# Optimization experiments

Hardware: AMD Instinct MI355X
Metric: run time of the kernel (lower is better)

Reference implementation:

```python
import jax, jax.numpy as jnp
import numpy as np

BN_EPS = 1e-5

def setup_inputs() -> dict:
    key = jax.random.key(0)
    k1, k2, k3 = jax.random.split(key, 3)
    B, C, H, W = 8, 96, 56, 56
    Cout = 2 * C  # must equal 2*C for the BatchNorm in the original module
    x = jax.random.normal(k1, (B, C, H, W), dtype=jnp.float32)
    conv_w = jax.random.normal(k2, (Cout, 2 * C), dtype=jnp.float32) * (1.0 / np.sqrt(2 * C))
    conv_b = jax.random.normal(k3, (Cout,), dtype=jnp.float32) * 0.01
    gamma = jnp.ones((Cout,), dtype=jnp.float32)
    beta = jnp.zeros((Cout,), dtype=jnp.float32)
    return {"x": x, "conv_w": conv_w, "conv_b": conv_b, "gamma": gamma, "beta": beta}

def _forward(x, conv_w, conv_b, gamma, beta):
    B, C, H, W = x.shape
    # b c h w -> b n c, n = H*W
    q = x.reshape(B, C, H * W).transpose(0, 2, 1)
    # unscaled self-attention (q == k == v == tokens)
    att = jnp.einsum('bnc,bmc->bnm', q, q)          # [B, N, N]
    att = jax.nn.softmax(att, axis=-1)
    att = jnp.einsum('bnm,bmc->bnc', att, q)        # [B, N, C]
    att = att.transpose(0, 2, 1).reshape(B, C, H, W)
    # max-relative: x_j = max(0, x - att) since x_j starts at zeros
    x_j = jnp.maximum(x - att, 0.0)
    cat = jnp.concatenate([x, x_j], axis=1)          # [B, 2C, H, W]
    # 1x1 conv
    y = jnp.einsum('bchw,oc->bohw', cat, conv_w) + conv_b[None, :, None, None]
    # BatchNorm2d in training mode: biased batch stats over (B, H, W)
    mean = jnp.mean(y, axis=(0, 2, 3), keepdims=True)
    var = jnp.var(y, axis=(0, 2, 3), keepdims=True)
    y = (y - mean) * jax.lax.rsqrt(var + BN_EPS)
    y = y * gamma[None, :, None, None] + beta[None, :, None, None]
    # torch nn.GELU default is exact (erf) GELU
    return jax.nn.gelu(y, approximate=False)

def reference(x, conv_w, conv_b, gamma, beta):
    return _forward(x, conv_w, conv_b, gamma, beta)
```

## Files before the change

kernel.cpp:

```cpp
#include <hip/hip_runtime.h>
#include <hip/hip_bf16.h>

#define B_    8
#define C_    96
#define N_    3136
#define COUT_ 192
#define NTOK_ 25088
#define BN_EPS 1e-5f

#define CROW 200
#define BNC  (B_ * N_ * C_)
#define NSPLIT 3
#define NT98  98

#define K2_V_OFF 6144
#define K2_BUFSZ 14336

typedef __hip_bfloat16 bf16;
typedef unsigned short u16;
typedef unsigned int u32;
typedef __attribute__((ext_vector_type(8))) short short8;
typedef __attribute__((ext_vector_type(16))) float f32x16;

__device__ __forceinline__ u16 f2bf(float f) {
    union { __hip_bfloat16 h; u16 u; } cv;
    cv.h = __float2bfloat16(f);
    return cv.u;
}
__device__ __forceinline__ float bf2f(u16 v) {
    union { u16 u; __hip_bfloat16 h; } cv;
    cv.u = v;
    return __bfloat162float(cv.h);
}
__device__ __forceinline__ u32 packbf2(float lo, float hi) {
    return ((u32)f2bf(hi) << 16) | (u32)f2bf(lo);
}

__device__ __forceinline__ void gload_lds16(const void* g, void* l) {
    __builtin_amdgcn_global_load_lds((const __attribute__((address_space(1))) void*)g,
                                     (__attribute__((address_space(3))) void*)l,
                                     16, 0, 0);
}

__device__ __forceinline__ size_t foff(int t, int kc) {
    return ((size_t)t * 6 + kc) << 9;
}

__global__ __launch_bounds__(256) void transpose_split(const float* __restrict__ x,
                                                       u16* __restrict__ xf_hi,
                                                       u16* __restrict__ xf_lo,
                                                       u16* __restrict__ xc_hi,
                                                       float* __restrict__ norm2) {
    __shared__ float tile[32][33];
    __shared__ float nrm[32];
    const int nb = blockIdx.x * 32;
    const int cb = blockIdx.y * 32;
    const int b  = blockIdx.z;
    const int tid = threadIdx.x;
    const int tx = tid & 31;
    const int ty = tid >> 5;
    if (tid < 32) nrm[tid] = 0.0f;
    float psum = 0.0f;
#pragma unroll
    for (int r = 0; r < 32; r += 8) {
        size_t idx = ((size_t)b * C_ + cb + ty + r) * N_ + nb + tx;
        float v = x[idx];
        tile[ty + r][tx] = v;
        xc_hi[idx] = f2bf(v);
        psum = fmaf(v, v, psum);
    }
    __syncthreads();
    atomicAdd(&nrm[tx], psum);

    {
        const int item  = tid & 127;
        const int is_lo = tid >> 7;
        const int kc_i  = item >> 6;
        const int l     = item & 63;
        const int kcg   = (cb >> 4) + kc_i;
        union { u16 a[8]; short8 v8; } o;
#pragma unroll
        for (int j = 0; j < 8; j++) {
            float v = tile[kc_i * 16 + ((l >> 5) * 8) + j][l & 31];
            u16 h = f2bf(v);
            o.a[j] = is_lo ? f2bf(v - bf2f(h)) : h;
        }
        u16* dst = (is_lo ? xf_lo : xf_hi) +
                   ((size_t)b * NT98 * 6 << 9) + foff(nb >> 5, kcg) + l * 8;
        *(short8*)dst = o.v8;
    }
    __syncthreads();
    if (tid < 32)
        atomicAdd(&norm2[(size_t)b * N_ + nb + tid], nrm[tid]);
}

__global__ __launch_bounds__(256) void cast_w(const float* __restrict__ w,
                                              u16* __restrict__ wf_hi,
                                              u16* __restrict__ wf_lo) {
    int i = blockIdx.x * 256 + threadIdx.x;
    if (i >= COUT_ * 2 * C_) return;
    float v = w[i];
    u16 h  = f2bf(v);
    u16 lo = f2bf(v - bf2f(h));
    int o = i / (2 * C_), c = i % (2 * C_);
    int mt = o >> 5, lrow = o & 31;
    int ks = c >> 4, hi8 = (c >> 3) & 1, j = c & 7;
    size_t d = ((size_t)(mt * 12 + ks) * 64 + hi8 * 32 + lrow) * 8 + j;
    wf_hi[d] = h;
    wf_lo[d] = lo;
}

__global__ __launch_bounds__(256) void norm_max(const float* __restrict__ norm2,
                                                int* __restrict__ maxbits) {
    const int tid = blockIdx.x * 256 + threadIdx.x;
    float m = 0.0f;
    for (int i = tid; i < NTOK_; i += gridDim.x * 256) m = fmaxf(m, norm2[i]);
#pragma unroll
    for (int d = 1; d < 64; d <<= 1) m = fmaxf(m, __shfl_xor(m, d));
    if ((threadIdx.x & 63) == 0) atomicMax(maxbits, __float_as_int(m));
}

__global__ __launch_bounds__(256, 3) void flash_attn_mfma32(const u16* __restrict__ xf_hi,
                                                            const u16* __restrict__ xf_lo,
                                                            const u16* __restrict__ xc_hi,
                                                            const float* __restrict__ norm2,
                                                            const int* __restrict__ maxbits,
                                                            float* __restrict__ attT,
                                                            float* __restrict__ l_arr) {
    __shared__ __align__(16) char LDSU[2][K2_BUFSZ];
    const int b     = blockIdx.y;
    const int i0    = blockIdx.x * 128;
    const int split = blockIdx.z;
    const int kt0   = (NT98 * split) / NSPLIT;
    const int kt1   = (NT98 * (split + 1)) / NSPLIT;
    const int tid   = threadIdx.x;
    const int lane  = tid & 63;
    const int w     = tid >> 6;
    const int col   = lane & 31;
    const int g     = lane >> 5;

    const u16* fh = xf_hi + ((size_t)b * NT98 * 6 << 9);
    const u16* fl = xf_lo + ((size_t)b * NT98 * 6 << 9);
    const u16* vh = xc_hi + (size_t)b * C_ * N_;

    u32 loff[4], dofs[4];
#pragma unroll
    for (int j = 0; j < 4; j++) {
        int s = w + 4 * j;
        if (s >= 14) { loff[j] = 0; dofs[j] = 0; continue; }
        if (s < 6) {
            loff[j] = (u32)(s * 1024 + lane * 16);
            dofs[j] = (u32)(s * 1024);
        } else {
            int t = s - 6;
            int p = t * 64 + lane;
            int ch = p / 5, c = p % 5;
            if (c > 3) c = 3;
            loff[j] = (ch < 96) ? (u32)(ch * (N_ * 2) + c * 16) : 0u;
            dofs[j] = (u32)(K2_V_OFF + t * 1024);
        }
    }

    int qt = blockIdx.x * 4 + w;
    if (qt > NT98 - 1) qt = NT98 - 1;
    const int qrow  = i0 + w * 32 + col;
    const int qrowc = qrow < N_ ? qrow : N_ - 1;
    short8 qh[6], ql[6];
#pragma unroll
    for (int kc = 0; kc < 6; kc++) {
        qh[kc] = *(const short8*)&fh[foff(qt, kc) + lane * 8];
        ql[kc] = *(const short8*)&fl[foff(qt, kc) + lane * 8];
    }
    const float maxn2 = __int_as_float(*maxbits);
    const float m_i   = sqrtf(norm2[(size_t)b * N_ + qrowc] * maxn2);
    float l_acc = 0.0f;
    f32x16 O0 = {0}, O1 = {0}, O2 = {0};

    auto stage = [&](int nbuf, int kt) {
        const u32 ktK = (u32)kt * 6144u;
        const u32 ktV = (u32)kt * 64u;
#pragma unroll
        for (int j = 0; j < 4; j++) {
            int s = w + 4 * j;
            if (s >= 14) break;
            const char* sb = (s < 6) ? (const char*)fh + ktK
                                     : (const char*)vh + ktV;
            gload_lds16(sb + loff[j], (char*)&LDSU[nbuf][0] + dofs[j]);
        }
    };

    stage(0, kt0);
    __syncthreads();

    const int g16 = g * 16;
    int buf = 0;
    for (int kt = kt0; kt < kt1; kt++) {
        if (kt + 1 < kt1) stage(buf ^ 1, kt + 1);

        const char* Lb = (const char*)&LDSU[buf][0];

        short8 kl[6];
#pragma unroll
        for (int kc = 0; kc < 6; kc++)
            kl[kc] = *(const short8*)&fl[foff(kt, kc) + lane * 8];

        f32x16 S = {0};
        __builtin_amdgcn_s_setprio(1);
#pragma unroll
        for (int kc = 0; kc < 6; kc++) {
            short8 kh = *(const short8*)(Lb + kc * 1024 + lane * 16);
            S = __builtin_amdgcn_mfma_f32_32x32x16_bf16(kh, ql[kc], S, 0, 0, 0);
            S = __builtin_amdgcn_mfma_f32_32x32x16_bf16(kl[kc], qh[kc], S, 0, 0, 0);
            S = __builtin_amdgcn_mfma_f32_32x32x16_bf16(kh, qh[kc], S, 0, 0, 0);
        }
        __builtin_amdgcn_s_setprio(0);

        float p[16];
#pragma unroll
        for (int r = 0; r < 16; r++) {
            p[r] = __expf(S[r] - m_i);
            l_acc += p[r];
        }
        u32 w8[8];
#pragma unroll
        for (int q = 0; q < 8; q++) w8[q] = packbf2(p[2 * q], p[2 * q + 1]);

        __builtin_amdgcn_s_setprio(1);
#pragma unroll
        for (int kc = 0; kc < 2; kc++) {
            const int qb = kc * 4;
            u32 a0 = w8[qb + 0], a1 = w8[qb + 1];
            u32 a2 = w8[qb + 2], a3 = w8[qb + 3];
            u32 s0 = __shfl_xor((int)a0, 32), s1 = __shfl_xor((int)a1, 32);
            u32 s2 = __shfl_xor((int)a2, 32), s3 = __shfl_xor((int)a3, 32);
            union { short8 v; u32 u[4]; } Bf;
            Bf.u[0] = g ? s2 : a0;
            Bf.u[1] = g ? s3 : a1;
            Bf.u[2] = g ? a2 : s0;
            Bf.u[3] = g ? a3 : s1;
            const int vo = K2_V_OFF + col * 80 + kc * 32 + g16;
            short8 v0 = *(const short8*)(Lb + vo);
            short8 v1 = *(const short8*)(Lb + vo + 2560);
            short8 v2 = *(const short8*)(Lb + vo + 5120);
            O0 = __builtin_amdgcn_mfma_f32_32x32x16_bf16(v0, Bf.v, O0, 0, 0, 0);
            O1 = __builtin_amdgcn_mfma_f32_32x32x16_bf16(v1, Bf.v, O1, 0, 0, 0);
            O2 = __builtin_amdgcn_mfma_f32_32x32x16_bf16(v2, Bf.v, O2, 0, 0, 0);
        }
        __builtin_amdgcn_s_setprio(0);

        __syncthreads();
        buf ^= 1;
    }

    if (qrow < N_) {
        float* ab = attT + (size_t)b * C_ * N_ + qrow;
#pragma unroll
        for (int r = 0; r < 16; r++) {
            int c = (r & 3) + 8 * (r >> 2) + 4 * g;
            atomicAdd(&ab[(size_t)(c)      * N_], O0[r]);
            atomicAdd(&ab[(size_t)(c + 32) * N_], O1[r]);
            atomicAdd(&ab[(size_t)(c + 64) * N_], O2[r]);
        }
        float l_tot = l_acc + __shfl_xor(l_acc, 32);
        if (g == 0) atomicAdd(&l_arr[(size_t)b * N_ + qrow], l_tot);
    }
}

__global__ __launch_bounds__(128, 3) void conv_mfma(const float* __restrict__ x,
                                                    const float* __restrict__ attT,
                                                    const float* __restrict__ l_arr,
                                                    const u16* __restrict__ wf_hi,
                                                    const u16* __restrict__ wf_lo,
                                                    const float* __restrict__ convb,
                                                    float* __restrict__ y) {
    __shared__ u16 ch[32 * CROW];
    __shared__ u16 cl[32 * CROW];
    __shared__ float invl[32];
    const int b   = blockIdx.x / (N_ / 32);
    const int n0  = (blockIdx.x % (N_ / 32)) * 32;
    const int tid = threadIdx.x;

    if (tid < 32) invl[tid] = 1.0f / l_arr[(size_t)b * N_ + n0 + tid];
    __syncthreads();

    const float* xb = x    + (size_t)b * C_ * N_ + n0;
    const float* ab = attT + (size_t)b * C_ * N_ + n0;
    for (int e = tid; e < 32 * C_; e += 128) {
        int c = e >> 5, t = e & 31;
        float xv = xb[(size_t)c * N_ + t];
        float au = ab[(size_t)c * N_ + t];
        float xj = fmaxf(xv - au * invl[t], 0.0f);
        u16 h1 = f2bf(xv);
        ch[t * CROW + c] = h1;
        cl[t * CROW + c] = f2bf(xv - bf2f(h1));
        u16 h2 = f2bf(xj);
        ch[t * CROW + C_ + c] = h2;
        cl[t * CROW + C_ + c] = f2bf(xj - bf2f(h2));
    }
    __syncthreads();

    const int lane = tid & 63;
    const int w    = tid >> 6;
    const int col  = lane & 31;
    const int g    = lane >> 5;
    const int m0   = w * 3;

    f32x16 A[3] = {{0}, {0}, {0}};
#pragma unroll
    for (int ks = 0; ks < 12; ks++) {
        const int k0 = ks * 16;
        short8 bh = *(const short8*)&ch[col * CROW + k0 + g * 8];
        short8 bl = *(const short8*)&cl[col * CROW + k0 + g * 8];
#pragma unroll
        for (int mt = 0; mt < 3; mt++) {
            const size_t wo = (size_t)((m0 + mt) * 12 + ks) * 512 + lane * 8;
            short8 ah = *(const short8*)&wf_hi[wo];
            short8 al = *(const short8*)&wf_lo[wo];
            A[mt] = __builtin_amdgcn_mfma_f32_32x32x16_bf16(ah, bl, A[mt], 0, 0, 0);
            A[mt] = __builtin_amdgcn_mfma_f32_32x32x16_bf16(al, bh, A[mt], 0, 0, 0);
            A[mt] = __builtin_amdgcn_mfma_f32_32x32x16_bf16(ah, bh, A[mt], 0, 0, 0);
        }
    }

    float* yb = y + (size_t)b * COUT_ * N_ + n0 + col;
#pragma unroll
    for (int mt = 0; mt < 3; mt++)
#pragma unroll
        for (int r = 0; r < 16; r++) {
            int o = (m0 + mt) * 32 + (r & 3) + 8 * (r >> 2) + 4 * g;
            yb[(size_t)o * N_] = A[mt][r] + convb[o];
        }
}

__global__ __launch_bounds__(256) void bn_partial(const float* __restrict__ y,
                                                  float* __restrict__ pb) {
    const int o   = blockIdx.x;
    const int b   = blockIdx.y;
    const int tid = threadIdx.x;
    float s = 0.0f, q = 0.0f;
    const float4* p = (const float4*)(y + (size_t)(b * COUT_ + o) * N_);
    for (int i = tid; i < N_ / 4; i += 256) {
        float4 v = p[i];
        s += v.x + v.y + v.z + v.w;
        q += v.x * v.x + v.y * v.y + v.z * v.z + v.w * v.w;
    }
#pragma unroll
    for (int d = 1; d < 64; d <<= 1) {
        s += __shfl_xor(s, d);
        q += __shfl_xor(q, d);
    }
    __shared__ float wss[4], wqq[4];
    if ((tid & 63) == 0) { wss[tid >> 6] = s; wqq[tid >> 6] = q; }
    __syncthreads();
    if (tid == 0) {
        pb[b * COUT_ + o]                = wss[0] + wss[1] + wss[2] + wss[3];
        pb[B_ * COUT_ + b * COUT_ + o]   = wqq[0] + wqq[1] + wqq[2] + wqq[3];
    }
}

__global__ __launch_bounds__(192) void bn_finish(const float* __restrict__ pb,
                                                 const float* __restrict__ gamma,
                                                 const float* __restrict__ beta,
                                                 float* __restrict__ ss) {
    const int o = threadIdx.x;
    float s = 0.0f, q = 0.0f;
#pragma unroll
    for (int b = 0; b < B_; b++) {
        s += pb[b * COUT_ + o];
        q += pb[B_ * COUT_ + b * COUT_ + o];
    }
    const float invn = 1.0f / (float)NTOK_;
    float mean = s * invn;
    float var  = q * invn - mean * mean;
    float sc   = gamma[o] * rsqrtf(var + BN_EPS);
    ss[o]         = sc;
    ss[COUT_ + o] = beta[o] - mean * sc;
}

__global__ __launch_bounds__(256) void bn_gelu_out(const float* __restrict__ y,
                                                   const float* __restrict__ ss,
                                                   float* __restrict__ out) {
    const int total4 = (B_ * COUT_ * N_) / 4;
    int i = blockIdx.x * 256 + threadIdx.x;
    if (i >= total4) return;
    int base = i * 4;
    int o = (base / N_) % COUT_;
    float sc = ss[o], sh = ss[COUT_ + o];
    float4 v = *(const float4*)&y[base];
    float u0 = fmaf(v.x, sc, sh), u1 = fmaf(v.y, sc, sh);
    float u2 = fmaf(v.z, sc, sh), u3 = fmaf(v.w, sc, sh);
    const float k = 0.70710678118654752f;
    float4 g;
    g.x = 0.5f * u0 * (1.0f + erff(u0 * k));
    g.y = 0.5f * u1 * (1.0f + erff(u1 * k));
    g.z = 0.5f * u2 * (1.0f + erff(u2 * k));
    g.w = 0.5f * u3 * (1.0f + erff(u3 * k));
    *(float4*)&out[base] = g;
}

extern "C" void kernel_launch(void* const* d_in, const int* in_sizes, int n_in,
                              void* d_out, int out_size, void* d_ws, size_t ws_size,
                              hipStream_t stream) {
    const float* x     = (const float*)d_in[0];
    const float* w     = (const float*)d_in[1];
    const float* cb    = (const float*)d_in[2];
    const float* gamma = (const float*)d_in[3];
    const float* beta  = (const float*)d_in[4];

    u16* xf_hi = (u16*)d_ws;
    u16* xf_lo = xf_hi + (size_t)BNC;
    u16* xc_hi = xf_lo + (size_t)BNC;
    float* attT  = (float*)(xc_hi + (size_t)BNC);
    u16* wf_hi = (u16*)(attT + (size_t)BNC);
    u16* wf_lo = wf_hi + COUT_ * 2 * C_;
    float* y     = (float*)(wf_lo + COUT_ * 2 * C_);
    float* ss    = y + (size_t)B_ * COUT_ * N_;
    float* l_arr = ss + 2 * COUT_;
    float* norm2 = l_arr + NTOK_;
    int*   maxb  = (int*)(norm2 + NTOK_);
    float* pb    = attT;

    hipMemsetAsync(l_arr, 0, (2 * NTOK_) * sizeof(float) + sizeof(int), stream);
    hipMemsetAsync(attT, 0, (size_t)BNC * sizeof(float), stream);

    transpose_split<<<dim3(N_ / 32, C_ / 32, B_), 256, 0, stream>>>(x, xf_hi, xf_lo, xc_hi, norm2);
    cast_w<<<dim3((COUT_ * 2 * C_ + 255) / 256), 256, 0, stream>>>(w, wf_hi, wf_lo);
    norm_max<<<dim3(25), 256, 0, stream>>>(norm2, maxb);
    flash_attn_mfma32<<<dim3((N_ + 127) / 128, B_, NSPLIT), 256, 0, stream>>>(
        xf_hi, xf_lo, xc_hi, norm2, maxb, attT, l_arr);
    conv_mfma<<<dim3(B_ * (N_ / 32)), 128, 0, stream>>>(x, attT, l_arr, wf_hi, wf_lo, cb, y);
    bn_partial<<<dim3(COUT_, B_), 256, 0, stream>>>(y, pb);
    bn_finish<<<dim3(1), 192, 0, stream>>>(pb, gamma, beta, ss);
    bn_gelu_out<<<dim3((B_ * COUT_ * N_ / 4 + 255) / 256), 256, 0, stream>>>(y, ss, (float*)d_out);
}
```

Baseline: 206.3 us.

## Stream-K split attention tiles evenly across a fixed grid of blocks

Replaces the fixed 3-way key split per query block with a stream-K style schedule. 768 blocks each take a contiguous range of (query-block, key-tile) work items and flush partial results by atomics whenever the query block changes. The goal is to balance work across CUs and remove the tail wave left by the old 25x8x3 grid. In exchange some blocks do extra Q reloads and extra atomic flushes, and the per-tile div/mod indexing adds scalar overhead.

```diff
diff --git a/kernel.cpp b/kernel.cpp
--- a/kernel.cpp
+++ b/kernel.cpp
@@ -10,8 +10,11 @@
 
 #define CROW 200
 #define BNC  (B_ * N_ * C_)
-#define NSPLIT 3
 #define NT98  98
+
+#define NPAIR 200
+#define TILES_TOTAL (NPAIR * NT98)
+#define NBLK2 768
 
 #define K2_V_OFF 6144
 #define K2_BUFSZ 14336
@@ -128,20 +131,16 @@
                                                             float* __restrict__ attT,
                                                             float* __restrict__ l_arr) {
     __shared__ __align__(16) char LDSU[2][K2_BUFSZ];
-    const int b     = blockIdx.y;
-    const int i0    = blockIdx.x * 128;
-    const int split = blockIdx.z;
-    const int kt0   = (NT98 * split) / NSPLIT;
-    const int kt1   = (NT98 * (split + 1)) / NSPLIT;
-    const int tid   = threadIdx.x;
-    const int lane  = tid & 63;
-    const int w     = tid >> 6;
-    const int col   = lane & 31;
-    const int g     = lane >> 5;
-
-    const u16* fh = xf_hi + ((size_t)b * NT98 * 6 << 9);
-    const u16* fl = xf_lo + ((size_t)b * NT98 * 6 << 9);
-    const u16* vh = xc_hi + (size_t)b * C_ * N_;
+    const int tid  = threadIdx.x;
+    const int lane = tid & 63;
+    const int w    = tid >> 6;
+    const int col  = lane & 31;
+    const int g    = lane >> 5;
+    const int g16  = g * 16;
+
+    const int beta = blockIdx.x;
+    const int t0 = (int)(((long long)beta * TILES_TOTAL) / NBLK2);
+    const int t1 = (int)(((long long)(beta + 1) * TILES_TOTAL) / NBLK2);
 
     u32 loff[4], dofs[4];
 #pragma unroll
@@ -161,42 +160,74 @@
         }
     }
 
-    int qt = blockIdx.x * 4 + w;
-    if (qt > NT98 - 1) qt = NT98 - 1;
-    const int qrow  = i0 + w * 32 + col;
-    const int qrowc = qrow < N_ ? qrow : N_ - 1;
+    const float maxn2 = __int_as_float(*maxbits);
+
+    int pr = -1, b = 0, qrow = 0;
+    const u16* fh = xf_hi;
+    const u16* fl = xf_lo;
     short8 qh[6], ql[6];
-#pragma unroll
-    for (int kc = 0; kc < 6; kc++) {
-        qh[kc] = *(const short8*)&fh[foff(qt, kc) + lane * 8];
-        ql[kc] = *(const short8*)&fl[foff(qt, kc) + lane * 8];
-    }
-    const float maxn2 = __int_as_float(*maxbits);
-    const float m_i   = sqrtf(norm2[(size_t)b * N_ + qrowc] * maxn2);
-    float l_acc = 0.0f;
-    f32x16 O0 = {0}, O1 = {0}, O2 = {0};
-
-    auto stage = [&](int nbuf, int kt) {
-        const u32 ktK = (u32)kt * 6144u;
-        const u32 ktV = (u32)kt * 64u;
+    float m_i = 0.0f, l_acc = 0.0f;
+    f32x16 O0, O1, O2;
+
+    auto load_pair = [&](int np) {
+        pr = np;
+        b = pr / 25;
+        int qb = pr % 25;
+        fh = xf_hi + ((size_t)b * NT98 * 6 << 9);
+        fl = xf_lo + ((size_t)b * NT98 * 6 << 9);
+        int qt = qb * 4 + w;
+        if (qt > NT98 - 1) qt = NT98 - 1;
+        qrow = qb * 128 + w * 32 + col;
+        const int qrowc = qrow < N_ ? qrow : N_ - 1;
+#pragma unroll
+        for (int kc = 0; kc < 6; kc++) {
+            qh[kc] = *(const short8*)&fh[foff(qt, kc) + lane * 8];
+            ql[kc] = *(const short8*)&fl[foff(qt, kc) + lane * 8];
+        }
+        m_i = sqrtf(norm2[(size_t)b * N_ + qrowc] * maxn2);
+        l_acc = 0.0f;
+#pragma unroll
+        for (int i = 0; i < 16; i++) { O0[i] = 0.0f; O1[i] = 0.0f; O2[i] = 0.0f; }
+    };
+
+    auto flush = [&]() {
+        if (qrow < N_) {
+            float* ab = attT + (size_t)b * C_ * N_ + qrow;
+#pragma unroll
+            for (int r = 0; r < 16; r++) {
+                int c = (r & 3) + 8 * (r >> 2) + 4 * g;
+                atomicAdd(&ab[(size_t)(c)      * N_], O0[r]);
+                atomicAdd(&ab[(size_t)(c + 32) * N_], O1[r]);
+                atomicAdd(&ab[(size_t)(c + 64) * N_], O2[r]);
+            }
+            float l_tot = l_acc + __shfl_xor(l_acc, 32);
+            if (g == 0) atomicAdd(&l_arr[(size_t)b * N_ + qrow], l_tot);
+        }
+    };
+
+    auto stage = [&](int nbuf, int t) {
+        const int tb = (t / NT98) / 25;
+        const int kt = t % NT98;
+        const char* sK = (const char*)(xf_hi + ((size_t)tb * NT98 * 6 << 9)) + (u32)kt * 6144u;
+        const char* sV = (const char*)(xc_hi + (size_t)tb * C_ * N_) + (u32)kt * 64u;
 #pragma unroll
         for (int j = 0; j < 4; j++) {
             int s = w + 4 * j;
             if (s >= 14) break;
-            const char* sb = (s < 6) ? (const char*)fh + ktK
-                                     : (const char*)vh + ktV;
+            const char* sb = (s < 6) ? sK : sV;
             gload_lds16(sb + loff[j], (char*)&LDSU[nbuf][0] + dofs[j]);
         }
     };
 
-    stage(0, kt0);
-    __syncthreads();
-
-    const int g16 = g * 16;
+    load_pair(t0 / NT98);
+    stage(0, t0);
+    __syncthreads();
+
     int buf = 0;
-    for (int kt = kt0; kt < kt1; kt++) {
-        if (kt + 1 < kt1) stage(buf ^ 1, kt + 1);
-
+    for (int t = t0; t < t1; t++) {
+        if (t + 1 < t1) stage(buf ^ 1, t + 1);
+
+        const int kt = t % NT98;
         const char* Lb = (const char*)&LDSU[buf][0];
 
         short8 kl[6];
@@ -228,9 +259,9 @@
         __builtin_amdgcn_s_setprio(1);
 #pragma unroll
         for (int kc = 0; kc < 2; kc++) {
-            const int qb = kc * 4;
-            u32 a0 = w8[qb + 0], a1 = w8[qb + 1];
-            u32 a2 = w8[qb + 2], a3 = w8[qb + 3];
+            const int qb2 = kc * 4;
+            u32 a0 = w8[qb2 + 0], a1 = w8[qb2 + 1];
+            u32 a2 = w8[qb2 + 2], a3 = w8[qb2 + 3];
             u32 s0 = __shfl_xor((int)a0, 32), s1 = __shfl_xor((int)a1, 32);
             u32 s2 = __shfl_xor((int)a2, 32), s3 = __shfl_xor((int)a3, 32);
             union { short8 v; u32 u[4]; } Bf;
@@ -250,20 +281,13 @@
 
         __syncthreads();
         buf ^= 1;
-    }
-
-    if (qrow < N_) {
-        float* ab = attT + (size_t)b * C_ * N_ + qrow;
-#pragma unroll
-        for (int r = 0; r < 16; r++) {
-            int c = (r & 3) + 8 * (r >> 2) + 4 * g;
-            atomicAdd(&ab[(size_t)(c)      * N_], O0[r]);
-            atomicAdd(&ab[(size_t)(c + 32) * N_], O1[r]);
-            atomicAdd(&ab[(size_t)(c + 64) * N_], O2[r]);
-        }
-        float l_tot = l_acc + __shfl_xor(l_acc, 32);
-        if (g == 0) atomicAdd(&l_arr[(size_t)b * N_ + qrow], l_tot);
-    }
+
+        if (t + 1 < t1) {
+            int np = (t + 1) / NT98;
+            if (np != pr) { flush(); load_pair(np); }
+        }
+    }
+    flush();
 }
 
 __global__ __launch_bounds__(128, 3) void conv_mfma(const float* __restrict__ x,
@@ -426,7 +450,7 @@
     transpose_split<<<dim3(N_ / 32, C_ / 32, B_), 256, 0, stream>>>(x, xf_hi, xf_lo, xc_hi, norm2);
     cast_w<<<dim3((COUT_ * 2 * C_ + 255) / 256), 256, 0, stream>>>(w, wf_hi, wf_lo);
     norm_max<<<dim3(25), 256, 0, stream>>>(norm2, maxb);
-    flash_attn_mfma32<<<dim3((N_ + 127) / 128, B_, NSPLIT), 256, 0, stream>>>(
+    flash_attn_mfma32<<<dim3(NBLK2), 256, 0, stream>>>(
         xf_hi, xf_lo, xc_hi, norm2, maxb, attT, l_arr);
     conv_mfma<<<dim3(B_ * (N_ / 32)), 128, 0, stream>>>(x, attT, l_arr, wf_hi, wf_lo, cb, y);
     bn_partial<<<dim3(COUT_, B_), 256, 0, stream>>>(y, pb);
```

Measured after the change: 209.2 us. No clear change (+1.4%).
